# Kernel optimization log

Hardware: AMD Instinct MI355X
Metric: run time of the kernel (lower is better)

The kernel has to match this reference:

```python
import jax, jax.numpy as jnp
import numpy as np

NUM_ITERATIONS = 3


def squash(v, axis=-1):
    sq = jnp.sum(v * v, axis=axis, keepdims=True)
    scale = sq / (1.0 + sq)
    return scale * v / jnp.sqrt(sq)


def setup_inputs() -> dict:
    key = jax.random.key(0)
    k1, k2 = jax.random.split(key)
    B, N, IN, OUT, CAPS = 512, 4608, 16, 32, 32
    x = jax.random.normal(k1, (B, N, IN), dtype=jnp.float32)
    # torch.rand -> uniform [0, 1)
    route_weights = jax.random.uniform(k2, (N, IN, OUT), dtype=jnp.float32)
    return {"x": x, "route_weights": route_weights, "num_capsules": CAPS}


def reference(x, route_weights, num_capsules):
    # x: [B, N, IN], route_weights: [N, IN, OUT]
    u_hat = jnp.einsum('bnk,nkl->bnl', x, route_weights)  # [B, N, OUT]
    N = x.shape[1]
    b = jnp.zeros((N, num_capsules), dtype=u_hat.dtype)  # routing logits [N, CAPS]
    v = None
    for it in range(NUM_ITERATIONS):
        c = jax.nn.softmax(b, axis=-1)                     # [N, CAPS]
        s = jnp.einsum('bnk,nc->bck', u_hat, c)            # [B, CAPS, OUT]
        v = squash(s, axis=-1)                             # [B, CAPS, OUT]
        if it < NUM_ITERATIONS - 1:
            b = b + jnp.einsum('bnk,bck->nc', u_hat, v)    # agreement, reduced over batch
    return v
```

## Files before the change

### kernel.cpp

```cpp
#include <hip/hip_runtime.h>


#define NB 512
#define KTOT 73728
#define OUTC 32
#define NCAPS 32

#define KSPLIT 16
#define KCHUNK (KTOT / KSPLIT)
#define KT 256
#define NTILES (KCHUNK / KT)
#define RPW 4
#define NWAVES 4
#define RPB (RPW * NWAVES)
#define NRG (NB / RPB)
#define LSTR 33

__global__ __launch_bounds__(256) void zero_ws(float* __restrict__ S) {
    int i = blockIdx.x * 256 + threadIdx.x;
    if (i < NB * OUTC) S[i] = 0.0f;
}

__global__ __launch_bounds__(256, 2) void gemm_splitk(
        const float* __restrict__ x, const float* __restrict__ w,
        float* __restrict__ S) {
    __shared__ float wlds[KT * LSTR];
    const int t = threadIdx.x;
    const int lane = t & 63;
    const int wave = t >> 6;
    const int row0 = blockIdx.x * RPB + wave * RPW;
    const size_t kbase = (size_t)blockIdx.y * KCHUNK;

    float acc[RPW][OUTC];
#pragma unroll
    for (int r = 0; r < RPW; ++r)
#pragma unroll
        for (int c = 0; c < OUTC; ++c) acc[r][c] = 0.0f;

    const float* xp[RPW];
#pragma unroll
    for (int r = 0; r < RPW; ++r)
        xp[r] = x + (size_t)(row0 + r) * KTOT + kbase;

    for (int tile = 0; tile < NTILES; ++tile) {
        const float4* wv = (const float4*)(w + (kbase + (size_t)tile * KT) * OUTC);
#pragma unroll
        for (int j = 0; j < 8; ++j) {
            int f = j * 256 + t;
            int kk = f >> 3;
            int g  = f & 7;
            float4 v = wv[f];
            float* dst = &wlds[kk * LSTR + g * 4];
            dst[0] = v.x; dst[1] = v.y; dst[2] = v.z; dst[3] = v.w;
        }
        __syncthreads();

#pragma unroll
        for (int i = 0; i < KT / 64; ++i) {
            const int kl = lane + i * 64;
            float xr[RPW];
#pragma unroll
            for (int r = 0; r < RPW; ++r)
                xr[r] = xp[r][tile * KT + kl];
            const float* wrow = &wlds[kl * LSTR];
#pragma unroll
            for (int c = 0; c < OUTC; ++c) {
                const float wc = wrow[c];
#pragma unroll
                for (int r = 0; r < RPW; ++r)
                    acc[r][c] = fmaf(xr[r], wc, acc[r][c]);
            }
        }
        __syncthreads();
    }

#pragma unroll
    for (int r = 0; r < RPW; ++r) {
        float myv = 0.0f;
#pragma unroll
        for (int c = 0; c < OUTC; ++c) {
            float v = acc[r][c];
            v += __shfl_xor(v, 32, 64);
            v += __shfl_xor(v, 16, 64);
            v += __shfl_xor(v, 8, 64);
            v += __shfl_xor(v, 4, 64);
            v += __shfl_xor(v, 2, 64);
            v += __shfl_xor(v, 1, 64);
            if (lane == c) myv = v;
        }
        if (lane < OUTC)
            atomicAdd(&S[(size_t)(row0 + r) * OUTC + lane], myv);
    }
}

__global__ __launch_bounds__(64) void finalize(const float* __restrict__ S,
                                               float* __restrict__ out) {
    const int b = blockIdx.x;
    const int t = threadIdx.x;
    const int k = t & 31;
    const int half = t >> 5;
    float s = S[b * OUTC + k] * (1.0f / 32.0f);
    float sq = s * s;
    sq += __shfl_xor(sq, 16, 64);
    sq += __shfl_xor(sq, 8, 64);
    sq += __shfl_xor(sq, 4, 64);
    sq += __shfl_xor(sq, 2, 64);
    sq += __shfl_xor(sq, 1, 64);
    float scale = sq / ((1.0f + sq) * sqrtf(sq));
    float v = s * scale;
    float* orow = out + (size_t)b * (NCAPS * OUTC);
#pragma unroll
    for (int j = 0; j < 16; ++j) {
        int c = half + j * 2;
        orow[c * OUTC + k] = v;
    }
}

extern "C" void kernel_launch(void* const* d_in, const int* in_sizes, int n_in,
                              void* d_out, int out_size, void* d_ws, size_t ws_size,
                              hipStream_t stream) {
    const float* x = (const float*)d_in[0];
    const float* w = (const float*)d_in[1];
    float* out = (float*)d_out;
    float* S = (float*)d_ws;

    hipLaunchKernelGGL(zero_ws, dim3((NB * OUTC + 255) / 256), dim3(256), 0, stream, S);
    hipLaunchKernelGGL(gemm_splitk, dim3(NRG, KSPLIT), dim3(256), 0, stream, x, w, S);
    hipLaunchKernelGGL(finalize, dim3(NB), dim3(64), 0, stream, S, out);
}
```

Before: 261.3 us.

## Restructure split-K GEMM with float4 x loads, transposed W tile, and partial-sum buffer

Raises the K split from 16 to 64 and halves the tile to 128. Each wave now covers two row groups with 32 lanes each, and every lane loads float4 chunks of x. W is stored transposed in LDS so that each lane reads a float4 per output column, and the reduction inside each half-wave is one shuffle step shorter. When the workspace is large enough, atomics and the zeroing kernel are replaced by per-split partial buffers that the finalize kernel reduces. This targets x load efficiency, atomic contention and occupancy, at the cost of more partial-sum traffic and non-coalesced scalar W loads.

```diff
diff --git a/kernel.cpp b/kernel.cpp
--- a/kernel.cpp
+++ b/kernel.cpp
@@ -6,30 +6,40 @@
 #define OUTC 32
 #define NCAPS 32
 
-#define KSPLIT 16
+#define KSPLIT 64
 #define KCHUNK (KTOT / KSPLIT)
-#define KT 256
+#define KT 128
 #define NTILES (KCHUNK / KT)
-#define RPW 4
+#define NQ (KT / 4)
+#define RPW 2
 #define NWAVES 4
-#define RPB (RPW * NWAVES)
+#define RPB (NWAVES * 2 * RPW)
 #define NRG (NB / RPB)
-#define LSTR 33
+#define KSTR (KT + 4)
+
+#define WS_NEED ((size_t)KSPLIT * NB * OUTC * 4)
 
 __global__ __launch_bounds__(256) void zero_ws(float* __restrict__ S) {
     int i = blockIdx.x * 256 + threadIdx.x;
     if (i < NB * OUTC) S[i] = 0.0f;
 }
 
-__global__ __launch_bounds__(256, 2) void gemm_splitk(
+template <bool PART>
+__global__ __launch_bounds__(256) void gemm_k(
         const float* __restrict__ x, const float* __restrict__ w,
         float* __restrict__ S) {
-    __shared__ float wlds[KT * LSTR];
+    __shared__ float wlds[OUTC * KSTR];
     const int t = threadIdx.x;
     const int lane = t & 63;
+    const int l32 = lane & 31;
+    const int half = lane >> 5;
     const int wave = t >> 6;
-    const int row0 = blockIdx.x * RPB + wave * RPW;
-    const size_t kbase = (size_t)blockIdx.y * KCHUNK;
+    const int bx = blockIdx.x, by = blockIdx.y;
+    const int row0 = bx * RPB + wave * (2 * RPW) + half * RPW;
+    const size_t kbase = (size_t)by * KCHUNK;
+
+    const int sc = t & 31;
+    const int sh = t >> 5;
 
     float acc[RPW][OUTC];
 #pragma unroll
@@ -37,38 +47,41 @@
 #pragma unroll
         for (int c = 0; c < OUTC; ++c) acc[r][c] = 0.0f;
 
-    const float* xp[RPW];
+    const float4* xq[RPW];
 #pragma unroll
     for (int r = 0; r < RPW; ++r)
-        xp[r] = x + (size_t)(row0 + r) * KTOT + kbase;
+        xq[r] = (const float4*)(x + (size_t)(row0 + r) * KTOT + kbase);
 
     for (int tile = 0; tile < NTILES; ++tile) {
-        const float4* wv = (const float4*)(w + (kbase + (size_t)tile * KT) * OUTC);
+        float4 xv[RPW];
 #pragma unroll
-        for (int j = 0; j < 8; ++j) {
-            int f = j * 256 + t;
-            int kk = f >> 3;
-            int g  = f & 7;
-            float4 v = wv[f];
-            float* dst = &wlds[kk * LSTR + g * 4];
-            dst[0] = v.x; dst[1] = v.y; dst[2] = v.z; dst[3] = v.w;
+        for (int r = 0; r < RPW; ++r)
+            xv[r] = xq[r][tile * NQ + l32];
+
+#pragma unroll
+        for (int jj = 0; jj < 4; ++jj) {
+            int kq = jj * 8 + sh;
+            int kk = 4 * kq;
+            const float* wg = w + (kbase + (size_t)tile * KT + kk) * OUTC + sc;
+            float w0 = wg[0];
+            float w1 = wg[OUTC];
+            float w2 = wg[2 * OUTC];
+            float w3 = wg[3 * OUTC];
+            *(float4*)&wlds[sc * KSTR + kk] = make_float4(w0, w1, w2, w3);
         }
         __syncthreads();
 
 #pragma unroll
-        for (int i = 0; i < KT / 64; ++i) {
-            const int kl = lane + i * 64;
-            float xr[RPW];
+        for (int c = 0; c < OUTC; ++c) {
+            float4 wv = *(const float4*)&wlds[c * KSTR + 4 * l32];
 #pragma unroll
-            for (int r = 0; r < RPW; ++r)
-                xr[r] = xp[r][tile * KT + kl];
-            const float* wrow = &wlds[kl * LSTR];
-#pragma unroll
-            for (int c = 0; c < OUTC; ++c) {
-                const float wc = wrow[c];
-#pragma unroll
-                for (int r = 0; r < RPW; ++r)
-                    acc[r][c] = fmaf(xr[r], wc, acc[r][c]);
+            for (int r = 0; r < RPW; ++r) {
+                float a = acc[r][c];
+                a = fmaf(xv[r].x, wv.x, a);
+                a = fmaf(xv[r].y, wv.y, a);
+                a = fmaf(xv[r].z, wv.z, a);
+                a = fmaf(xv[r].w, wv.w, a);
+                acc[r][c] = a;
             }
         }
         __syncthreads();
@@ -80,26 +93,39 @@
 #pragma unroll
         for (int c = 0; c < OUTC; ++c) {
             float v = acc[r][c];
-            v += __shfl_xor(v, 32, 64);
             v += __shfl_xor(v, 16, 64);
             v += __shfl_xor(v, 8, 64);
             v += __shfl_xor(v, 4, 64);
             v += __shfl_xor(v, 2, 64);
             v += __shfl_xor(v, 1, 64);
-            if (lane == c) myv = v;
+            if (l32 == c) myv = v;
         }
-        if (lane < OUTC)
-            atomicAdd(&S[(size_t)(row0 + r) * OUTC + lane], myv);
+        const int row = row0 + r;
+        if (PART)
+            S[((size_t)by * NB + row) * OUTC + l32] = myv;
+        else
+            atomicAdd(&S[(size_t)row * OUTC + l32], myv);
     }
 }
 
-__global__ __launch_bounds__(64) void finalize(const float* __restrict__ S,
-                                               float* __restrict__ out) {
+template <bool PART>
+__global__ __launch_bounds__(64) void finalize_k(const float* __restrict__ S,
+                                                 float* __restrict__ out) {
     const int b = blockIdx.x;
     const int t = threadIdx.x;
     const int k = t & 31;
-    const int half = t >> 5;
-    float s = S[b * OUTC + k] * (1.0f / 32.0f);
+    const int h = t >> 5;
+    float s;
+    if (PART) {
+        float a = 0.0f;
+#pragma unroll
+        for (int i = 0; i < KSPLIT / 2; ++i)
+            a += S[((size_t)(h * (KSPLIT / 2) + i) * NB + b) * OUTC + k];
+        a += __shfl_xor(a, 32, 64);
+        s = a * (1.0f / 32.0f);
+    } else {
+        s = S[(size_t)b * OUTC + k] * (1.0f / 32.0f);
+    }
     float sq = s * s;
     sq += __shfl_xor(sq, 16, 64);
     sq += __shfl_xor(sq, 8, 64);
@@ -110,10 +136,8 @@
     float v = s * scale;
     float* orow = out + (size_t)b * (NCAPS * OUTC);
 #pragma unroll
-    for (int j = 0; j < 16; ++j) {
-        int c = half + j * 2;
-        orow[c * OUTC + k] = v;
-    }
+    for (int j = 0; j < 16; ++j)
+        orow[(h + j * 2) * OUTC + k] = v;
 }
 
 extern "C" void kernel_launch(void* const* d_in, const int* in_sizes, int n_in,
@@ -124,7 +148,15 @@
     float* out = (float*)d_out;
     float* S = (float*)d_ws;
 
-    hipLaunchKernelGGL(zero_ws, dim3((NB * OUTC + 255) / 256), dim3(256), 0, stream, S);
-    hipLaunchKernelGGL(gemm_splitk, dim3(NRG, KSPLIT), dim3(256), 0, stream, x, w, S);
-    hipLaunchKernelGGL(finalize, dim3(NB), dim3(64), 0, stream, S, out);
+    if (ws_size >= WS_NEED) {
+        hipLaunchKernelGGL((gemm_k<true>), dim3(NRG, KSPLIT), dim3(256), 0, stream,
+                           x, w, S);
+        hipLaunchKernelGGL((finalize_k<true>), dim3(NB), dim3(64), 0, stream, S, out);
+    } else {
+        hipLaunchKernelGGL(zero_ws, dim3((NB * OUTC + 255) / 256), dim3(256), 0,
+                           stream, S);
+        hipLaunchKernelGGL((gemm_k<false>), dim3(NRG, KSPLIT), dim3(256), 0, stream,
+                           x, w, S);
+        hipLaunchKernelGGL((finalize_k<false>), dim3(NB), dim3(64), 0, stream, S, out);
+    }
 }
```

Result: slower. 279.3 us (+6.9%).
